# Kernel optimization log

Measured on AMD Instinct MI355X. Metric: run time of the kernel, lower is better.

## Reference

```python
import jax, jax.numpy as jnp
import numpy as np

B, T, I, H = 512, 256, 256, 512


def _lstm(x, Wih, Whh, bih, bhh):
    # x: [B, T, I]; Wih: [4H, I]; Whh: [4H, H]; gate order i, f, g, o (torch)
    Bv = x.shape[0]
    Hv = Whh.shape[1]
    xg = jnp.einsum('bti,gi->btg', x, Wih) + bih + bhh  # [B, T, 4H] (input projections hoisted out of scan)
    xg = jnp.transpose(xg, (1, 0, 2))  # [T, B, 4H]
    h0 = jnp.zeros((Bv, Hv), x.dtype)
    c0 = jnp.zeros((Bv, Hv), x.dtype)

    def step(carry, gx):
        h, c = carry
        g = gx + h @ Whh.T  # [B, 4H]
        i, f, gg, o = jnp.split(g, 4, axis=-1)
        i = jax.nn.sigmoid(i)
        f = jax.nn.sigmoid(f)
        gg = jnp.tanh(gg)
        o = jax.nn.sigmoid(o)
        c = f * c + i * gg
        h = o * jnp.tanh(c)
        return (h, c), h

    _, hs = jax.lax.scan(step, (h0, c0), xg)  # hs: [T, B, H]
    return jnp.transpose(hs, (1, 0, 2))  # [B, T, H]


def _bn1d(x, gamma, beta, eps=1e-5):
    # torch BatchNorm1d on [N, C, L] in training mode: per-channel stats over (N, L), biased var
    m = jnp.mean(x, axis=(0, 2), keepdims=True)
    v = jnp.var(x, axis=(0, 2), keepdims=True)
    return (x - m) * jax.lax.rsqrt(v + eps) * gamma[None, :, None] + beta[None, :, None]


def setup_inputs() -> dict:
    key = jax.random.key(0)
    ks = jax.random.split(key, 14)
    s = 1.0 / np.sqrt(H)
    return {
        'x': jax.random.normal(ks[0], (B, T, I), jnp.float32),
        'Wih': jax.random.uniform(ks[1], (4 * H, I), jnp.float32, -s, s),
        'Whh': jax.random.uniform(ks[2], (4 * H, H), jnp.float32, -s, s),
        'bih': jax.random.uniform(ks[3], (4 * H,), jnp.float32, -s, s),
        'bhh': jax.random.uniform(ks[4], (4 * H,), jnp.float32, -s, s),
        'fc1_w': jax.random.uniform(ks[5], (32, H), jnp.float32, -s, s),
        'fc1_b': jax.random.uniform(ks[6], (32,), jnp.float32, -s, s),
        'fc2_w': jax.random.uniform(ks[7], (1, 32), jnp.float32, -0.17, 0.17),
        'fc2_b': jax.random.uniform(ks[8], (1,), jnp.float32, -0.17, 0.17),
        'bn1_g': jnp.ones((T,), jnp.float32),
        'bn1_b': jnp.zeros((T,), jnp.float32),
        'bn2_g': jnp.ones((T,), jnp.float32),
        'bn2_b': jnp.zeros((T,), jnp.float32),
    }


def reference(x, Wih, Whh, bih, bhh, fc1_w, fc1_b, fc2_w, fc2_b, bn1_g, bn1_b, bn2_g, bn2_b):
    lstm_out = _lstm(x, Wih, Whh, bih, bhh)  # [B, T, H]
    a = jnp.einsum('bth,oh->bto', lstm_out, fc1_w) + fc1_b  # [B, T, 32]
    a = jax.nn.leaky_relu(_bn1d(a, bn1_g, bn1_b), negative_slope=0.1)
    z = jnp.einsum('bto,po->btp', a, fc2_w) + fc2_b  # [B, T, 1]
    out = jax.nn.relu(_bn1d(z, bn2_g, bn2_b))
    return out
```

## Files before the change

kernel.cpp:

```cpp
#include <hip/hip_runtime.h>

#define BB 512
#define TT 256
#define II 256
#define HH 512

typedef __attribute__((ext_vector_type(8))) short bf16x8;
typedef __attribute__((ext_vector_type(4))) float f32x4;

__device__ __forceinline__ unsigned short f2bf(float f) {
  union { float f; unsigned u; } v; v.f = f;
  unsigned r = v.u + 0x7fffu + ((v.u >> 16) & 1u);
  return (unsigned short)(r >> 16);
}

#define OFF_CNT   0
#define OFF_HSWZ  4096
#define OFF_XSWZ  1052672ULL
#define OFF_HIST  68161536ULL
#define ZERO_WORDS 263168

__global__ void zero_k(unsigned* __restrict__ p, int n) {
  int i = blockIdx.x * blockDim.x + threadIdx.x;
  if (i < n) p[i] = 0u;
}

__global__ __launch_bounds__(256) void prep_x(const float* __restrict__ x,
                                              unsigned char* __restrict__ ws) {
  __shared__ unsigned short xs[16][264];
  const int t = blockIdx.x >> 5, rc = blockIdx.x & 31;
  const int tid = threadIdx.x;
  {
    const int r = tid >> 4, seg = tid & 15;
    const float* src = x + ((size_t)(rc * 16 + r) * TT + t) * II + seg * 16;
    const float4* s4 = (const float4*)src;
#pragma unroll
    for (int q = 0; q < 4; ++q) {
      float4 v = s4[q];
      xs[r][seg * 16 + q * 4 + 0] = f2bf(v.x);
      xs[r][seg * 16 + q * 4 + 1] = f2bf(v.y);
      xs[r][seg * 16 + q * 4 + 2] = f2bf(v.z);
      xs[r][seg * 16 + q * 4 + 3] = f2bf(v.w);
    }
  }
  __syncthreads();
  const int lane = tid & 63;
  const int row16 = lane & 15, koff = (lane >> 4) * 8;
#pragma unroll
  for (int kc = tid >> 6; kc < 8; kc += 4) {
    union { unsigned short h[8]; uint4 v; } pk;
#pragma unroll
    for (int j = 0; j < 8; ++j) pk.h[j] = xs[row16][kc * 32 + koff + j];
    *(uint4*)(ws + OFF_XSWZ + (size_t)(t * 8 + kc) * 32768u +
              ((size_t)rc * 64 + lane) * 16) = pk.v;
  }
}

__global__ __launch_bounds__(512, 2) void lstm_persist(
    const float* __restrict__ Wih, const float* __restrict__ Whh,
    const float* __restrict__ bih, const float* __restrict__ bhh,
    unsigned char* __restrict__ ws)
{
  const int gid = blockIdx.x;
  const int group = gid & 7;
  const int m = gid >> 3;
  const int tid = threadIdx.x;
  const int wv = tid >> 6, lane = tid & 63;
  const int mb = wv & 3, kh = wv >> 2;
  const int lq = lane >> 4, ln = lane & 15;

  int* flags_g = (int*)(ws + OFF_CNT + (size_t)group * 512);
  unsigned char* xswz  = ws + OFF_XSWZ;
  unsigned char* hswz0 = ws + OFF_HSWZ;
  unsigned char* hswz1 = ws + OFF_HSWZ + 524288;
  unsigned char* hist  = ws + OFF_HIST;

  __shared__ int step_flag;
  if (tid == 0) step_flag = 0;

  bf16x8 Wf[12][4];
#pragma unroll
  for (int kk = 0; kk < 12; ++kk) {
    const int kb = (kh * 12 + kk) * 32 + lq * 8;
#pragma unroll
    for (int nt = 0; nt < 4; ++nt) {
      const int gcol = nt * 512 + m * 16 + ln;
      const float* s = (kb < 256) ? (Wih + (size_t)gcol * 256 + kb)
                                  : (Whh + (size_t)gcol * 512 + (kb - 256));
      bf16x8 w;
#pragma unroll
      for (int j = 0; j < 8; ++j) w[j] = (short)f2bf(s[j]);
      Wf[kk][nt] = w;
    }
  }

  float bia[4];
#pragma unroll
  for (int nt = 0; nt < 4; ++nt) {
    int gcol = nt * 512 + m * 16 + ln;
    bia[nt] = bih[gcol] + bhh[gcol];
  }

  __shared__ float g_s[64 * 68];
  __shared__ float h_s[64 * 17];

  const size_t aoff = ((size_t)(group * 4 + mb) * 64 + lane) * 16;
  float creg[4] = {0.f, 0.f, 0.f, 0.f};
  const f32x4 zero4 = {0.f, 0.f, 0.f, 0.f};

#pragma unroll 1
  for (int t = 0; t < 256; ++t) {
    unsigned char* hrd = (t & 1) ? hswz1 : hswz0;
    unsigned char* hwr = (t & 1) ? hswz0 : hswz1;

    f32x4 acc[4] = {zero4, zero4, zero4, zero4};

    if (kh == 0) {
#pragma unroll
      for (int kk = 0; kk < 8; ++kk) {
        bf16x8 a = *(const bf16x8*)(xswz + (size_t)(t * 8 + kk) * 32768u + aoff);
#pragma unroll
        for (int nt = 0; nt < 4; ++nt)
          acc[nt] = __builtin_amdgcn_mfma_f32_16x16x32_bf16(a, Wf[kk][nt], acc[nt], 0, 0, 0);
      }
    }

    if (t > 0) {
      if (kh == 1) {
        int iter = 0;
        for (;;) {
          int v = __hip_atomic_load(flags_g + (lane & 31), __ATOMIC_RELAXED,
                                    __HIP_MEMORY_SCOPE_AGENT);
          if (__all(v >= t)) break;
          if (++iter >= (1 << 17)) break;
          __builtin_amdgcn_s_sleep(1);
        }
        if (wv == 4)
          __hip_atomic_store(&step_flag, t, __ATOMIC_RELAXED,
                             __HIP_MEMORY_SCOPE_WORKGROUP);
      } else {
        int iter = 0;
        while (__hip_atomic_load(&step_flag, __ATOMIC_RELAXED,
                                 __HIP_MEMORY_SCOPE_WORKGROUP) < t
               && iter < (1 << 20)) {
          ++iter;
          __builtin_amdgcn_s_sleep(1);
        }
      }
      asm volatile("" ::: "memory");
    }

    if (kh == 0) {
      unsigned long long u0[4], u1[4];
#pragma unroll
      for (int p = 0; p < 4; ++p) {
        const unsigned long long* q =
            (const unsigned long long*)(hrd + (size_t)p * 32768u + aoff);
        u0[p] = __hip_atomic_load(q + 0, __ATOMIC_RELAXED, __HIP_MEMORY_SCOPE_AGENT);
        u1[p] = __hip_atomic_load(q + 1, __ATOMIC_RELAXED, __HIP_MEMORY_SCOPE_AGENT);
      }
#pragma unroll
      for (int kk = 0; kk < 4; ++kk) {
        union { unsigned long long q[2]; bf16x8 v; } u;
        u.q[0] = u0[kk]; u.q[1] = u1[kk];
#pragma unroll
        for (int nt = 0; nt < 4; ++nt)
          acc[nt] = __builtin_amdgcn_mfma_f32_16x16x32_bf16(u.v, Wf[8 + kk][nt], acc[nt], 0, 0, 0);
      }
    } else {
      unsigned long long u0[6], u1[6];
#pragma unroll
      for (int p = 0; p < 6; ++p) {
        const unsigned long long* q =
            (const unsigned long long*)(hrd + (size_t)(4 + p) * 32768u + aoff);
        u0[p] = __hip_atomic_load(q + 0, __ATOMIC_RELAXED, __HIP_MEMORY_SCOPE_AGENT);
        u1[p] = __hip_atomic_load(q + 1, __ATOMIC_RELAXED, __HIP_MEMORY_SCOPE_AGENT);
      }
#pragma unroll
      for (int kk = 0; kk < 12; ++kk) {
        const int slot = kk % 6;
        union { unsigned long long q[2]; bf16x8 v; } u;
        u.q[0] = u0[slot]; u.q[1] = u1[slot];
        if (kk < 6) {
          const unsigned long long* q =
              (const unsigned long long*)(hrd + (size_t)(10 + kk) * 32768u + aoff);
          u0[slot] = __hip_atomic_load(q + 0, __ATOMIC_RELAXED, __HIP_MEMORY_SCOPE_AGENT);
          u1[slot] = __hip_atomic_load(q + 1, __ATOMIC_RELAXED, __HIP_MEMORY_SCOPE_AGENT);
        }
#pragma unroll
        for (int nt = 0; nt < 4; ++nt)
          acc[nt] = __builtin_amdgcn_mfma_f32_16x16x32_bf16(u.v, Wf[kk][nt], acc[nt], 0, 0, 0);
      }
#pragma unroll
      for (int nt = 0; nt < 4; ++nt)
#pragma unroll
        for (int r = 0; r < 4; ++r)
          g_s[(mb * 16 + lq * 4 + r) * 68 + nt * 16 + ln] = acc[nt][r];
    }

    asm volatile("s_waitcnt lgkmcnt(0)" ::: "memory");
    __builtin_amdgcn_sched_barrier(0);
    __builtin_amdgcn_s_barrier();
    __builtin_amdgcn_sched_barrier(0);

    if (kh == 0) {
#pragma unroll
      for (int r = 0; r < 4; ++r) {
        const int rw = mb * 16 + lq * 4 + r;
        float gi = acc[0][r] + g_s[rw * 68 + ln]      + bia[0];
        float gf = acc[1][r] + g_s[rw * 68 + 16 + ln] + bia[1];
        float gg = acc[2][r] + g_s[rw * 68 + 32 + ln] + bia[2];
        float go = acc[3][r] + g_s[rw * 68 + 48 + ln] + bia[3];
        float iv = 1.f / (1.f + __expf(-gi));
        float fv = 1.f / (1.f + __expf(-gf));
        float gv = 1.f - 2.f / (__expf(2.f * gg) + 1.f);
        float ov = 1.f / (1.f + __expf(-go));
        float cv = fv * creg[r] + iv * gv;
        creg[r] = cv;
        h_s[rw * 17 + ln] = ov * (1.f - 2.f / (__expf(2.f * cv) + 1.f));
      }
      __builtin_amdgcn_sched_barrier(0);

      {
        int rc_l = tid >> 6;
        int rem = tid & 63;
        int lane_off = rem >> 1;
        int half = rem & 1;
        int l2 = (m & 1) * 32 + lane_off;
        int rowl = rc_l * 16 + (lane_off & 15);
        int jb = (lane_off >> 4) * 8 + half * 4;
        union { ushort4 s; unsigned long long q; } pk;
        pk.s = make_ushort4(f2bf(h_s[rowl * 17 + jb + 0]),
                            f2bf(h_s[rowl * 17 + jb + 1]),
                            f2bf(h_s[rowl * 17 + jb + 2]),
                            f2bf(h_s[rowl * 17 + jb + 3]));
        size_t off = ((size_t)((m >> 1) * 32 + group * 4 + rc_l) * 64 + l2) * 16 + half * 8;
        *(unsigned long long*)(hwr + off) = pk.q;
      }
    }
    __syncthreads();

    if (tid == 0)
      __hip_atomic_store(flags_g + m, t + 1, __ATOMIC_RELAXED,
                         __HIP_MEMORY_SCOPE_AGENT);

    if (tid < 256) {
      int row = tid >> 2, jb = (tid & 3) * 4;
      ushort4 hq = make_ushort4(f2bf(h_s[row * 17 + jb + 0]),
                                f2bf(h_s[row * 17 + jb + 1]),
                                f2bf(h_s[row * 17 + jb + 2]),
                                f2bf(h_s[row * 17 + jb + 3]));
      int b = group * 64 + row;
      *(ushort4*)(hist + ((size_t)(b * 256 + t) * 512 + m * 16 + jb) * 2) = hq;
    }
  }
}

__global__ __launch_bounds__(256) void e1_fc1(
    const float* __restrict__ fc1_w, const unsigned char* __restrict__ hist,
    float* __restrict__ a_out)
{
  const int tid = threadIdx.x, wv = tid >> 6, lane = tid & 63;
  const int lq = lane >> 4, ln = lane & 15;

  bf16x8 Bf[16][2];
#pragma unroll
  for (int kk = 0; kk < 16; ++kk) {
#pragma unroll
    for (int nt = 0; nt < 2; ++nt) {
      const float* s = fc1_w + (size_t)(nt * 16 + ln) * 512 + kk * 32 + lq * 8;
      bf16x8 w;
#pragma unroll
      for (int j = 0; j < 8; ++j) w[j] = (short)f2bf(s[j]);
      Bf[kk][nt] = w;
    }
  }

  const int rbase = blockIdx.x * 128 + wv * 32;
  const f32x4 zero4 = {0.f, 0.f, 0.f, 0.f};
  f32x4 acc[2][2] = {{zero4, zero4}, {zero4, zero4}};
#pragma unroll
  for (int kk = 0; kk < 16; ++kk) {
    bf16x8 a0 = *(const bf16x8*)(hist + ((size_t)(rbase + ln) * 512 + kk * 32 + lq * 8) * 2);
    bf16x8 a1 = *(const bf16x8*)(hist + ((size_t)(rbase + 16 + ln) * 512 + kk * 32 + lq * 8) * 2);
#pragma unroll
    for (int nt = 0; nt < 2; ++nt) {
      acc[0][nt] = __builtin_amdgcn_mfma_f32_16x16x32_bf16(a0, Bf[kk][nt], acc[0][nt], 0, 0, 0);
      acc[1][nt] = __builtin_amdgcn_mfma_f32_16x16x32_bf16(a1, Bf[kk][nt], acc[1][nt], 0, 0, 0);
    }
  }
#pragma unroll
  for (int mt = 0; mt < 2; ++mt)
#pragma unroll
    for (int nt = 0; nt < 2; ++nt)
#pragma unroll
      for (int r = 0; r < 4; ++r) {
        int row = rbase + mt * 16 + lq * 4 + r;
        a_out[(size_t)row * 32 + nt * 16 + ln] = acc[mt][nt][r];
      }
}

__global__ __launch_bounds__(256) void e2_head(
    const float* __restrict__ a_in, const float* __restrict__ fc1_b,
    const float* __restrict__ fc2_w, const float* __restrict__ fc2_b,
    const float* __restrict__ bn1_g, const float* __restrict__ bn1_b,
    const float* __restrict__ bn2_g, const float* __restrict__ bn2_b,
    float* __restrict__ out)
{
  const int t = blockIdx.x, tid = threadIdx.x;
  __shared__ float fb[32], fw[32];
  __shared__ float red[4][2], red2[4][2];
  if (tid < 32) { fb[tid] = fc1_b[tid]; fw[tid] = fc2_w[tid]; }
  __syncthreads();

  float va[2][32];
  float s1 = 0.f, s2 = 0.f;
#pragma unroll
  for (int rr = 0; rr < 2; ++rr) {
    int b = tid * 2 + rr;
    const float* p = a_in + ((size_t)b * 256 + t) * 32;
#pragma unroll
    for (int o = 0; o < 32; ++o) {
      float v = p[o] + fb[o];
      va[rr][o] = v;
      s1 += v; s2 += v * v;
    }
  }
#pragma unroll
  for (int off = 32; off > 0; off >>= 1) {
    s1 += __shfl_down(s1, off);
    s2 += __shfl_down(s2, off);
  }
  if ((tid & 63) == 0) { red[tid >> 6][0] = s1; red[tid >> 6][1] = s2; }
  __syncthreads();
  float tot1 = red[0][0] + red[1][0] + red[2][0] + red[3][0];
  float tot2 = red[0][1] + red[1][1] + red[2][1] + red[3][1];
  float m1 = tot1 * (1.f / 16384.f);
  float v1 = tot2 * (1.f / 16384.f) - m1 * m1;
  float sc1 = bn1_g[t] * rsqrtf(v1 + 1e-5f);
  float sh1 = bn1_b[t];

  float z[2];
  float zs1 = 0.f, zs2 = 0.f;
#pragma unroll
  for (int rr = 0; rr < 2; ++rr) {
    float acc = fc2_b[0];
#pragma unroll
    for (int o = 0; o < 32; ++o) {
      float av = (va[rr][o] - m1) * sc1 + sh1;
      av = (av > 0.f) ? av : 0.1f * av;
      acc += av * fw[o];
    }
    z[rr] = acc; zs1 += acc; zs2 += acc * acc;
  }
#pragma unroll
  for (int off = 32; off > 0; off >>= 1) {
    zs1 += __shfl_down(zs1, off);
    zs2 += __shfl_down(zs2, off);
  }
  if ((tid & 63) == 0) { red2[tid >> 6][0] = zs1; red2[tid >> 6][1] = zs2; }
  __syncthreads();
  float zt1 = red2[0][0] + red2[1][0] + red2[2][0] + red2[3][0];
  float zt2 = red2[0][1] + red2[1][1] + red2[2][1] + red2[3][1];
  float m2 = zt1 * (1.f / 512.f);
  float v2 = zt2 * (1.f / 512.f) - m2 * m2;
  float sc2 = bn2_g[t] * rsqrtf(v2 + 1e-5f);
  float sh2 = bn2_b[t];
#pragma unroll
  for (int rr = 0; rr < 2; ++rr) {
    int b = tid * 2 + rr;
    float res = (z[rr] - m2) * sc2 + sh2;
    out[(size_t)b * 256 + t] = (res > 0.f) ? res : 0.f;
  }
}

extern "C" void kernel_launch(void* const* d_in, const int* in_sizes, int n_in,
                              void* d_out, int out_size, void* d_ws, size_t ws_size,
                              hipStream_t stream) {
  const float* x    = (const float*)d_in[0];
  const float* Wih  = (const float*)d_in[1];
  const float* Whh  = (const float*)d_in[2];
  const float* bih  = (const float*)d_in[3];
  const float* bhh  = (const float*)d_in[4];
  const float* fc1w = (const float*)d_in[5];
  const float* fc1b = (const float*)d_in[6];
  const float* fc2w = (const float*)d_in[7];
  const float* fc2b = (const float*)d_in[8];
  const float* b1g  = (const float*)d_in[9];
  const float* b1b  = (const float*)d_in[10];
  const float* b2g  = (const float*)d_in[11];
  const float* b2b  = (const float*)d_in[12];
  unsigned char* ws = (unsigned char*)d_ws;
  float* out = (float*)d_out;
  float* a_buf = (float*)(ws + OFF_XSWZ);

  zero_k<<<1028, 256, 0, stream>>>((unsigned*)ws, ZERO_WORDS);
  prep_x<<<8192, 256, 0, stream>>>(x, ws);
  lstm_persist<<<256, 512, 0, stream>>>(Wih, Whh, bih, bhh, ws);
  e1_fc1<<<1024, 256, 0, stream>>>(fc1w, ws + OFF_HIST, a_buf);
  e2_head<<<256, 256, 0, stream>>>(a_buf, fc1b, fc2w, fc2b, b1g, b1b, b2g, b2b, out);
}
```

Measured before the change: 1.576 ms.

## Use inline-asm coherent dwordx4 loads with staged waits in LSTM recurrence

New measurement: 1.678 ms. 1.06x slower.

```diff
diff --git a/kernel.cpp b/kernel.cpp
--- a/kernel.cpp
+++ b/kernel.cpp
@@ -13,6 +13,16 @@
   unsigned r = v.u + 0x7fffu + ((v.u >> 16) & 1u);
   return (unsigned short)(r >> 16);
 }
+
+#define LD4_SC(d0,d1,d2,d3,p0,p1,p2,p3,WAITSTR)                      \
+  asm volatile(                                                       \
+    "global_load_dwordx4 %0, %4, off sc0 sc1\n\t"                    \
+    "global_load_dwordx4 %1, %5, off sc0 sc1\n\t"                    \
+    "global_load_dwordx4 %2, %6, off sc0 sc1\n\t"                    \
+    "global_load_dwordx4 %3, %7, off sc0 sc1" WAITSTR                \
+    : "=&v"(d0), "=&v"(d1), "=&v"(d2), "=&v"(d3)                     \
+    : "v"(p0), "v"(p1), "v"(p2), "v"(p3)                             \
+    : "memory")
 
 #define OFF_CNT   0
 #define OFF_HSWZ  4096
@@ -150,46 +160,57 @@
       asm volatile("" ::: "memory");
     }
 
+    const unsigned char* hbase = hrd + aoff;
     if (kh == 0) {
-      unsigned long long u0[4], u1[4];
-#pragma unroll
-      for (int p = 0; p < 4; ++p) {
-        const unsigned long long* q =
-            (const unsigned long long*)(hrd + (size_t)p * 32768u + aoff);
-        u0[p] = __hip_atomic_load(q + 0, __ATOMIC_RELAXED, __HIP_MEMORY_SCOPE_AGENT);
-        u1[p] = __hip_atomic_load(q + 1, __ATOMIC_RELAXED, __HIP_MEMORY_SCOPE_AGENT);
-      }
-#pragma unroll
-      for (int kk = 0; kk < 4; ++kk) {
-        union { unsigned long long q[2]; bf16x8 v; } u;
-        u.q[0] = u0[kk]; u.q[1] = u1[kk];
-#pragma unroll
-        for (int nt = 0; nt < 4; ++nt)
-          acc[nt] = __builtin_amdgcn_mfma_f32_16x16x32_bf16(u.v, Wf[8 + kk][nt], acc[nt], 0, 0, 0);
+      bf16x8 h0, h1, h2, h3;
+      LD4_SC(h0, h1, h2, h3,
+             hbase + 0u * 32768u, hbase + 1u * 32768u,
+             hbase + 2u * 32768u, hbase + 3u * 32768u,
+             "\n\ts_waitcnt vmcnt(0)");
+#pragma unroll
+      for (int nt = 0; nt < 4; ++nt) {
+        acc[nt] = __builtin_amdgcn_mfma_f32_16x16x32_bf16(h0, Wf[8][nt], acc[nt], 0, 0, 0);
+        acc[nt] = __builtin_amdgcn_mfma_f32_16x16x32_bf16(h1, Wf[9][nt], acc[nt], 0, 0, 0);
+        acc[nt] = __builtin_amdgcn_mfma_f32_16x16x32_bf16(h2, Wf[10][nt], acc[nt], 0, 0, 0);
+        acc[nt] = __builtin_amdgcn_mfma_f32_16x16x32_bf16(h3, Wf[11][nt], acc[nt], 0, 0, 0);
       }
     } else {
-      unsigned long long u0[6], u1[6];
-#pragma unroll
-      for (int p = 0; p < 6; ++p) {
-        const unsigned long long* q =
-            (const unsigned long long*)(hrd + (size_t)(4 + p) * 32768u + aoff);
-        u0[p] = __hip_atomic_load(q + 0, __ATOMIC_RELAXED, __HIP_MEMORY_SCOPE_AGENT);
-        u1[p] = __hip_atomic_load(q + 1, __ATOMIC_RELAXED, __HIP_MEMORY_SCOPE_AGENT);
-      }
-#pragma unroll
-      for (int kk = 0; kk < 12; ++kk) {
-        const int slot = kk % 6;
-        union { unsigned long long q[2]; bf16x8 v; } u;
-        u.q[0] = u0[slot]; u.q[1] = u1[slot];
-        if (kk < 6) {
-          const unsigned long long* q =
-              (const unsigned long long*)(hrd + (size_t)(10 + kk) * 32768u + aoff);
-          u0[slot] = __hip_atomic_load(q + 0, __ATOMIC_RELAXED, __HIP_MEMORY_SCOPE_AGENT);
-          u1[slot] = __hip_atomic_load(q + 1, __ATOMIC_RELAXED, __HIP_MEMORY_SCOPE_AGENT);
-        }
-#pragma unroll
-        for (int nt = 0; nt < 4; ++nt)
-          acc[nt] = __builtin_amdgcn_mfma_f32_16x16x32_bf16(u.v, Wf[kk][nt], acc[nt], 0, 0, 0);
+      bf16x8 a0, a1, a2, a3, b0, b1, b2, b3, c0, c1, c2, c3;
+      LD4_SC(a0, a1, a2, a3,
+             hbase + 4u * 32768u, hbase + 5u * 32768u,
+             hbase + 6u * 32768u, hbase + 7u * 32768u, "");
+      LD4_SC(b0, b1, b2, b3,
+             hbase + 8u * 32768u, hbase + 9u * 32768u,
+             hbase + 10u * 32768u, hbase + 11u * 32768u,
+             "\n\ts_waitcnt vmcnt(4)");
+      __builtin_amdgcn_sched_barrier(0);
+#pragma unroll
+      for (int nt = 0; nt < 4; ++nt) {
+        acc[nt] = __builtin_amdgcn_mfma_f32_16x16x32_bf16(a0, Wf[0][nt], acc[nt], 0, 0, 0);
+        acc[nt] = __builtin_amdgcn_mfma_f32_16x16x32_bf16(a1, Wf[1][nt], acc[nt], 0, 0, 0);
+        acc[nt] = __builtin_amdgcn_mfma_f32_16x16x32_bf16(a2, Wf[2][nt], acc[nt], 0, 0, 0);
+        acc[nt] = __builtin_amdgcn_mfma_f32_16x16x32_bf16(a3, Wf[3][nt], acc[nt], 0, 0, 0);
+      }
+      LD4_SC(c0, c1, c2, c3,
+             hbase + 12u * 32768u, hbase + 13u * 32768u,
+             hbase + 14u * 32768u, hbase + 15u * 32768u,
+             "\n\ts_waitcnt vmcnt(4)");
+      __builtin_amdgcn_sched_barrier(0);
+#pragma unroll
+      for (int nt = 0; nt < 4; ++nt) {
+        acc[nt] = __builtin_amdgcn_mfma_f32_16x16x32_bf16(b0, Wf[4][nt], acc[nt], 0, 0, 0);
+        acc[nt] = __builtin_amdgcn_mfma_f32_16x16x32_bf16(b1, Wf[5][nt], acc[nt], 0, 0, 0);
+        acc[nt] = __builtin_amdgcn_mfma_f32_16x16x32_bf16(b2, Wf[6][nt], acc[nt], 0, 0, 0);
+        acc[nt] = __builtin_amdgcn_mfma_f32_16x16x32_bf16(b3, Wf[7][nt], acc[nt], 0, 0, 0);
+      }
+      asm volatile("s_waitcnt vmcnt(0)" ::: "memory");
+      __builtin_amdgcn_sched_barrier(0);
+#pragma unroll
+      for (int nt = 0; nt < 4; ++nt) {
+        acc[nt] = __builtin_amdgcn_mfma_f32_16x16x32_bf16(c0, Wf[8][nt], acc[nt], 0, 0, 0);
+        acc[nt] = __builtin_amdgcn_mfma_f32_16x16x32_bf16(c1, Wf[9][nt], acc[nt], 0, 0, 0);
+        acc[nt] = __builtin_amdgcn_mfma_f32_16x16x32_bf16(c2, Wf[10][nt], acc[nt], 0, 0, 0);
+        acc[nt] = __builtin_amdgcn_mfma_f32_16x16x32_bf16(c3, Wf[11][nt], acc[nt], 0, 0, 0);
       }
 #pragma unroll
       for (int nt = 0; nt < 4; ++nt)
@@ -197,11 +218,7 @@
         for (int r = 0; r < 4; ++r)
           g_s[(mb * 16 + lq * 4 + r) * 68 + nt * 16 + ln] = acc[nt][r];
     }
-
-    asm volatile("s_waitcnt lgkmcnt(0)" ::: "memory");
-    __builtin_amdgcn_sched_barrier(0);
-    __builtin_amdgcn_s_barrier();
-    __builtin_amdgcn_sched_barrier(0);
+    __syncthreads();
 
     if (kh == 0) {
 #pragma unroll
@@ -219,24 +236,20 @@
         creg[r] = cv;
         h_s[rw * 17 + ln] = ov * (1.f - 2.f / (__expf(2.f * cv) + 1.f));
       }
-      __builtin_amdgcn_sched_barrier(0);
-
-      {
-        int rc_l = tid >> 6;
-        int rem = tid & 63;
-        int lane_off = rem >> 1;
-        int half = rem & 1;
-        int l2 = (m & 1) * 32 + lane_off;
-        int rowl = rc_l * 16 + (lane_off & 15);
-        int jb = (lane_off >> 4) * 8 + half * 4;
-        union { ushort4 s; unsigned long long q; } pk;
-        pk.s = make_ushort4(f2bf(h_s[rowl * 17 + jb + 0]),
-                            f2bf(h_s[rowl * 17 + jb + 1]),
-                            f2bf(h_s[rowl * 17 + jb + 2]),
-                            f2bf(h_s[rowl * 17 + jb + 3]));
-        size_t off = ((size_t)((m >> 1) * 32 + group * 4 + rc_l) * 64 + l2) * 16 + half * 8;
-        *(unsigned long long*)(hwr + off) = pk.q;
-      }
+    }
+    __syncthreads();
+
+    if (tid < 128) {
+      int rc_l = tid >> 5;
+      int lane_off = tid & 31;
+      int l2 = (m & 1) * 32 + lane_off;
+      int rowl = rc_l * 16 + (lane_off & 15);
+      int jb = (lane_off >> 4) * 8;
+      union { unsigned short s[8]; uint4 v; } pk;
+#pragma unroll
+      for (int j = 0; j < 8; ++j) pk.s[j] = f2bf(h_s[rowl * 17 + jb + j]);
+      size_t off = ((size_t)((m >> 1) * 32 + group * 4 + rc_l) * 64 + l2) * 16;
+      *(uint4*)(hwr + off) = pk.v;
     }
     __syncthreads();
 
@@ -244,14 +257,13 @@
       __hip_atomic_store(flags_g + m, t + 1, __ATOMIC_RELAXED,
                          __HIP_MEMORY_SCOPE_AGENT);
 
-    if (tid < 256) {
-      int row = tid >> 2, jb = (tid & 3) * 4;
-      ushort4 hq = make_ushort4(f2bf(h_s[row * 17 + jb + 0]),
-                                f2bf(h_s[row * 17 + jb + 1]),
-                                f2bf(h_s[row * 17 + jb + 2]),
-                                f2bf(h_s[row * 17 + jb + 3]));
+    if (tid < 128) {
+      int row = tid >> 1, jb = (tid & 1) * 8;
+      union { unsigned short s[8]; uint4 v; } hq;
+#pragma unroll
+      for (int j = 0; j < 8; ++j) hq.s[j] = f2bf(h_s[row * 17 + jb + j]);
       int b = group * 64 + row;
-      *(ushort4*)(hist + ((size_t)(b * 256 + t) * 512 + m * 16 + jb) * 2) = hq;
+      *(uint4*)(hist + ((size_t)(b * 256 + t) * 512 + m * 16 + jb) * 2) = hq.v;
     }
   }
 }
```
